# Kernel tuning notes

Hardware: AMD Instinct MI355X
Metric: run time of the kernel (lower is better)

The kernel has to match this reference:

```python
import jax, jax.numpy as jnp
import numpy as np

# dims
H = 1024          # hidden_size
E = 2048          # d_inner = 2*H
NH = 32           # nheads = E/64
P = 64            # headdim
N = 128           # d_state
G = 1             # ngroups
K = 4             # d_conv
Q = 128           # SSD chunk length
FF = 4096         # intermediate_size
EPS = 1e-6        # rms_norm_eps
NEPS = 1e-5       # mamba gated-norm eps
CONV_DIM = E + 2 * G * N            # 2304
D_IN = 2 * E + 2 * G * N + NH       # 4384


def rmsnorm(x, w, eps):
    v = jnp.mean(x.astype(jnp.float32) ** 2, axis=-1, keepdims=True)
    return (x.astype(jnp.float32) * jax.lax.rsqrt(v + eps)).astype(x.dtype) * w


def segsum(x):
    # x: [..., T] -> [..., T, T] with out[i,j] = sum_{j<k<=i} x[k], -inf above diag
    T = x.shape[-1]
    cs = jnp.cumsum(x, axis=-1)
    s = cs[..., :, None] - cs[..., None, :]
    mask = jnp.tril(jnp.ones((T, T), dtype=bool))
    return jnp.where(mask, s, -jnp.inf)


def ssd(x, dt, A_log, B, C):
    # x:[b,l,nh,p], dt:[b,l,nh], B,C:[b,l,N] (ngroups=1, shared over heads)
    b, l, nh, p = x.shape
    A = -jnp.exp(A_log)                      # [nh]
    dA = dt * A                              # [b,l,nh]
    xd = x * dt[..., None]                   # discretized input
    c = l // Q
    xd = xd.reshape(b, c, Q, nh, p)
    dAc = dA.reshape(b, c, Q, nh).transpose(0, 3, 1, 2)   # [b,h,c,q]
    Bc = B.reshape(b, c, Q, N)
    Cc = C.reshape(b, c, Q, N)
    A_cs = jnp.cumsum(dAc, axis=-1)                        # [b,h,c,q]
    Lm = jnp.exp(segsum(dAc))                              # [b,h,c,q,q]
    # intra-chunk (diagonal blocks)
    Y_diag = jnp.einsum('bcqn,bcsn,bhcqs,bcshp->bcqhp', Cc, Bc, Lm, xd)
    # per-chunk final states
    decay_states = jnp.exp(A_cs[..., -1:] - A_cs)          # [b,h,c,q]
    states = jnp.einsum('bcqn,bhcq,bcqhp->bchpn', Bc, decay_states, xd)
    # inter-chunk recurrence (initial state = 0)
    A_last = jnp.pad(A_cs[..., -1], ((0, 0), (0, 0), (1, 0)))   # [b,h,c+1]
    decay_chunk = jnp.exp(segsum(A_last))                       # [b,h,c+1,c+1]
    states = jnp.concatenate([jnp.zeros_like(states[:, :1]), states], axis=1)
    new_states = jnp.einsum('bhzc,bchpn->bzhpn', decay_chunk, states)[:, :-1]
    Y_off = jnp.einsum('bcqn,bchpn,bhcq->bcqhp', Cc, new_states, jnp.exp(A_cs))
    return (Y_diag + Y_off).reshape(b, l, nh, p)


def mamba2(h, w_in, w_conv, b_conv, dt_bias, A_log, D, w_mnorm, w_out):
    b, l, _ = h.shape
    zxbcdt = h @ w_in.T                         # [b,l,D_IN]
    z, xBC, dt = jnp.split(zxbcdt, [E, E + CONV_DIM], axis=-1)
    # causal depthwise conv (kernel K) over channels of xBC
    pad = jnp.pad(xBC, ((0, 0), (K - 1, 0), (0, 0)))
    xBC = sum(pad[:, k:k + l, :] * w_conv[:, k] for k in range(K)) + b_conv
    xBC = jax.nn.silu(xBC)
    x, B, C = jnp.split(xBC, [E, E + G * N], axis=-1)
    dt = jax.nn.softplus(dt + dt_bias)          # [b,l,NH]
    xh = x.reshape(b, l, NH, P)
    y = ssd(xh, dt, A_log, B, C)
    y = y + D[None, None, :, None] * xh         # per-head skip
    y = y.reshape(b, l, E)
    y = rmsnorm(y * jax.nn.silu(z), w_mnorm, NEPS)   # gated RMSNorm
    return y @ w_out.T


def setup_inputs() -> dict:
    key = jax.random.key(0)
    ks = jax.random.split(key, 12)
    dt0 = jax.random.uniform(ks[0], (NH,), minval=0.001, maxval=0.1)
    dt_bias = dt0 + jnp.log(-jnp.expm1(-dt0))   # inverse softplus
    return {
        'hidden_states': jax.random.normal(ks[1], (2, 2048, H), dtype=jnp.float32),
        'w_ln1': jnp.ones((H,), jnp.float32),
        'w_in': 0.02 * jax.random.normal(ks[2], (D_IN, H), dtype=jnp.float32),
        'w_conv': 0.1 * jax.random.normal(ks[3], (CONV_DIM, K), dtype=jnp.float32),
        'b_conv': jnp.zeros((CONV_DIM,), jnp.float32),
        'dt_bias': dt_bias,
        'A_log': jnp.log(jax.random.uniform(ks[4], (NH,), minval=1.0, maxval=16.0)),
        'D': jnp.ones((NH,), jnp.float32),
        'w_mnorm': jnp.ones((E,), jnp.float32),
        'w_out': 0.02 * jax.random.normal(ks[5], (H, E), dtype=jnp.float32),
        'w_ln2': jnp.ones((H,), jnp.float32),
        'w_gate': 0.02 * jax.random.normal(ks[6], (FF, H), dtype=jnp.float32),
        'w_up': 0.02 * jax.random.normal(ks[7], (FF, H), dtype=jnp.float32),
        'w_down': 0.02 * jax.random.normal(ks[8], (H, FF), dtype=jnp.float32),
    }


def reference(hidden_states, w_ln1, w_in, w_conv, b_conv, dt_bias, A_log, D,
              w_mnorm, w_out, w_ln2, w_gate, w_up, w_down):
    residual = hidden_states
    h = rmsnorm(hidden_states, w_ln1, EPS)
    h = mamba2(h, w_in, w_conv, b_conv, dt_bias, A_log, D, w_mnorm, w_out)
    hidden = residual + h
    residual = hidden
    h = rmsnorm(hidden, w_ln2, EPS)
    h = (jax.nn.silu(h @ w_gate.T) * (h @ w_up.T)) @ w_down.T
    return residual + h
```

## Files before the change

kernel.cpp:

```cpp
#include <hip/hip_runtime.h>

#define DEV static __device__ __forceinline__

typedef short bf16x8 __attribute__((ext_vector_type(8)));
typedef float floatx4 __attribute__((ext_vector_type(4)));
typedef unsigned short ushort4v __attribute__((ext_vector_type(4)));
typedef unsigned short ushort8v __attribute__((ext_vector_type(8)));

DEV unsigned short f32_bf16(float f) {
  unsigned int u = __builtin_bit_cast(unsigned int, f);
  u = u + 0x7fffu + ((u >> 16) & 1u);
  return (unsigned short)(u >> 16);
}
DEV float bf2f(unsigned short u) {
  unsigned int v = ((unsigned int)u) << 16;
  return __builtin_bit_cast(float, v);
}
DEV float sigmoidf_(float x) { return 1.0f / (1.0f + __expf(-x)); }
DEV float siluf_(float x) { return x * sigmoidf_(x); }

#define GLD_LDS16(g, l)                                                              \
  __builtin_amdgcn_global_load_lds((const __attribute__((address_space(1))) void*)(g), \
                                   (__attribute__((address_space(3))) void*)(l), 16, 0, 0)

template <int MODE, int BN>
__global__ __launch_bounds__(256) void gemm128(
    const unsigned short* __restrict__ A, const unsigned short* __restrict__ B,
    void* __restrict__ Cv, const unsigned short* __restrict__ other,
    int K, int lda, int ldb, int ldc, long long bsA, long long bsB, long long bsC) {
  constexpr int NBG = BN / 64;
  constexpr int NJ = BN / 32;
  constexpr int BUFSZ = 4096 + BN * 32;
  __shared__ unsigned short S[3 * BUFSZ];
  A += (long long)blockIdx.z * bsA;
  B += (long long)blockIdx.z * bsB;
  const long long coff = (long long)blockIdx.z * bsC;
  const int tid = threadIdx.x;
  const int w = tid >> 6, lane = tid & 63;

  const int nbx = gridDim.x, nby = gridDim.y;
  const int GM = 4;
  int bid = blockIdx.y * nbx + blockIdx.x;
  int gid = bid / (GM * nbx);
  int rem = bid - gid * (GM * nbx);
  int gsz = min(GM, nby - gid * GM);
  int mtile = gid * GM + rem % gsz;
  int ntile = rem / gsz;
  const int m0 = mtile << 7, n0 = ntile * BN;

  const int srow = lane >> 2;
  const int schunk = ((lane & 3) ^ (srow & 3)) * 8;
  const unsigned short* ag0 = A + (long long)(m0 + w * 32 + srow) * lda + schunk;
  const unsigned short* ag1 = ag0 + (long long)16 * lda;
  const unsigned short* bgp[NBG];
#pragma unroll
  for (int ii = 0; ii < NBG; ++ii)
    bgp[ii] = B + (long long)(n0 + w * (BN / 4) + srow + 16 * ii) * ldb + schunk;

  auto STAGE = [&](int buf, int k0) {
    unsigned short* as_ = S + buf * BUFSZ;
    unsigned short* bs_ = as_ + 4096;
    GLD_LDS16(ag0 + k0, as_ + w * 1024 + lane * 8);
    GLD_LDS16(ag1 + k0, as_ + w * 1024 + lane * 8 + 512);
#pragma unroll
    for (int ii = 0; ii < NBG; ++ii)
      GLD_LDS16(bgp[ii] + k0, bs_ + w * (NBG * 512) + ii * 512 + lane * 8);
  };

  const int wr = (w >> 1) << 6;
  const int wc = (w & 1) * (BN / 2);
  const int fr = lane & 15;
  const int slot = (((lane >> 4) ^ (fr & 3))) << 3;
  const int r0 = (lane >> 4) << 2;

  floatx4 acc[4][NJ];
#pragma unroll
  for (int i = 0; i < 4; ++i)
#pragma unroll
    for (int j = 0; j < NJ; ++j) acc[i][j] = (floatx4){0.f, 0.f, 0.f, 0.f};

  const int nsteps = K >> 5;
  STAGE(0, 0);
  if (nsteps > 1) STAGE(1, 32);

  int cur = 0, nxt2 = 2;
  for (int t = 0; t < nsteps; ++t) {
    if (t < nsteps - 1) {
      if constexpr (NBG == 2) {
        asm volatile("s_waitcnt vmcnt(4)" ::: "memory");
      } else {
        asm volatile("s_waitcnt vmcnt(6)" ::: "memory");
      }
    } else {
      asm volatile("s_waitcnt vmcnt(0)" ::: "memory");
    }
    __builtin_amdgcn_s_barrier();
    __builtin_amdgcn_sched_barrier(0);
    if (t + 2 < nsteps) STAGE(nxt2, (t + 2) * 32);
    __builtin_amdgcn_sched_barrier(0);
    const unsigned short* Ab = S + cur * BUFSZ;
    const unsigned short* Bb = Ab + 4096;
    bf16x8 af[4], bf_[NJ];
#pragma unroll
    for (int i = 0; i < 4; ++i)
      af[i] = *(const bf16x8*)(Ab + (wr + i * 16 + fr) * 32 + slot);
#pragma unroll
    for (int j = 0; j < NJ; ++j)
      bf_[j] = *(const bf16x8*)(Bb + (wc + j * 16 + fr) * 32 + slot);
#pragma unroll
    for (int i = 0; i < 4; ++i)
#pragma unroll
      for (int j = 0; j < NJ; ++j)
        acc[i][j] = __builtin_amdgcn_mfma_f32_16x16x32_bf16(af[i], bf_[j], acc[i][j], 0, 0, 0);
    __builtin_amdgcn_sched_barrier(0);
    cur = (cur == 2) ? 0 : cur + 1;
    nxt2 = (nxt2 == 2) ? 0 : nxt2 + 1;
  }

  if constexpr (MODE == 0) {
#pragma unroll
    for (int i = 0; i < 4; ++i) {
#pragma unroll
      for (int j = 0; j < NJ; ++j) {
        long long base = (long long)(m0 + wr + i * 16 + r0) * ldc + (n0 + wc + j * 16 + fr);
#pragma unroll
        for (int r = 0; r < 4; ++r) {
          ((float*)Cv)[coff + base + (long long)r * ldc] = acc[i][j][r];
        }
      }
    }
  } else {
    constexpr int PAD = BN + 4;
    float* scr = (float*)S;
    const int row_l = tid >> 2;
    const int cch = (tid & 3) * 16;
    __syncthreads();
#pragma unroll
    for (int pass = 0; pass < 2; ++pass) {
      if ((w >> 1) == pass) {
#pragma unroll
        for (int i = 0; i < 4; ++i) {
#pragma unroll
          for (int j = 0; j < NJ; ++j) {
            int rl = i * 16 + r0;
            int col = wc + j * 16 + fr;
#pragma unroll
            for (int r = 0; r < 4; ++r) scr[(rl + r) * PAD + col] = acc[i][j][r];
          }
        }
      }
      __syncthreads();
      long long grow = m0 + pass * 64 + row_l;
      long long gbase = coff + grow * ldc + n0;
      const float* srow_p = scr + row_l * PAD;
#pragma unroll
      for (int k = 0; k < BN / 64; ++k) {
        int col = cch + k * 64;
        float v[16];
        *(float4*)&v[0] = *(const float4*)(srow_p + col);
        *(float4*)&v[4] = *(const float4*)(srow_p + col + 4);
        *(float4*)&v[8] = *(const float4*)(srow_p + col + 8);
        *(float4*)&v[12] = *(const float4*)(srow_p + col + 12);
        ushort8v o0, o1;
        if constexpr (MODE == 2) {
          ushort8v u0 = *(const ushort8v*)(other + gbase + col);
          ushort8v u1 = *(const ushort8v*)(other + gbase + col + 8);
#pragma unroll
          for (int e = 0; e < 8; ++e) o0[e] = f32_bf16(siluf_(v[e]) * bf2f(u0[e]));
#pragma unroll
          for (int e = 0; e < 8; ++e) o1[e] = f32_bf16(siluf_(v[8 + e]) * bf2f(u1[e]));
        } else {
#pragma unroll
          for (int e = 0; e < 8; ++e) o0[e] = f32_bf16(v[e]);
#pragma unroll
          for (int e = 0; e < 8; ++e) o1[e] = f32_bf16(v[8 + e]);
        }
        *(ushort8v*)((unsigned short*)Cv + gbase + col) = o0;
        *(ushort8v*)((unsigned short*)Cv + gbase + col + 8) = o1;
      }
      __syncthreads();
    }
  }
}

template <int WM>
__global__ __launch_bounds__(256) void gemm_small_nt(
    const unsigned short* __restrict__ A, const unsigned short* __restrict__ B,
    float* __restrict__ C, int M, int N, int K, int lda, int ldb, int ldc) {
  const int w = threadIdx.x >> 6;
  const int lane = threadIdx.x & 63;
  const int lm = lane & 15;
  const int ko = (lane >> 4) << 3;
  const int bn0 = blockIdx.x << 6;
  const int m_base = blockIdx.y * (WM * 64) + w * (WM * 16);

  const unsigned short* arow[WM];
#pragma unroll
  for (int i = 0; i < WM; ++i) arow[i] = A + (long long)(m_base + i * 16 + lm) * lda + ko;
  int nv = (N - bn0) >> 4;
  nv = nv > 4 ? 4 : nv;
  const unsigned short* brow[4];
#pragma unroll
  for (int j = 0; j < 4; ++j) {
    int nr = bn0 + j * 16 + lm;
    brow[j] = B + (long long)(j < nv ? nr : 0) * ldb + ko;
  }
  floatx4 acc[WM][4];
#pragma unroll
  for (int i = 0; i < WM; ++i)
#pragma unroll
    for (int j = 0; j < 4; ++j) acc[i][j] = (floatx4){0.f, 0.f, 0.f, 0.f};
  for (int k0 = 0; k0 < K; k0 += 32) {
    bf16x8 a[WM];
#pragma unroll
    for (int i = 0; i < WM; ++i) a[i] = *(const bf16x8*)(arow[i] + k0);
#pragma unroll
    for (int j = 0; j < 4; ++j) {
      if (j < nv) {
        bf16x8 b = *(const bf16x8*)(brow[j] + k0);
#pragma unroll
        for (int i = 0; i < WM; ++i)
          acc[i][j] = __builtin_amdgcn_mfma_f32_16x16x32_bf16(a[i], b, acc[i][j], 0, 0, 0);
      }
    }
  }
  const int r0 = (lane >> 4) << 2;
#pragma unroll
  for (int i = 0; i < WM; ++i)
#pragma unroll
    for (int j = 0; j < 4; ++j)
      if (j < nv) {
        int col = bn0 + j * 16 + lm;
        long long base = (long long)(m_base + i * 16 + r0) * ldc + col;
#pragma unroll
        for (int r = 0; r < 4; ++r) C[base + (long long)r * ldc] = acc[i][j][r];
      }
}

__global__ __launch_bounds__(256) void f32_to_bf16_k(const float* __restrict__ src,
                                                     unsigned short* __restrict__ dst,
                                                     long long n4) {
  long long i = (long long)blockIdx.x * 256 + threadIdx.x;
  if (i < n4) {
    float4 v = ((const float4*)src)[i];
    ushort4v o = {f32_bf16(v.x), f32_bf16(v.y), f32_bf16(v.z), f32_bf16(v.w)};
    ((ushort4v*)dst)[i] = o;
  }
}

__global__ __launch_bounds__(256) void zero_out_k(float* __restrict__ o, long long n) {
  long long i = (long long)blockIdx.x * 256 + threadIdx.x;
  if (i < n) o[i] = 0.f;
}

__global__ __launch_bounds__(256) void rmsnorm1024_bf16_k(const float* __restrict__ x,
                                                          const float* __restrict__ w,
                                                          unsigned short* __restrict__ out,
                                                          float eps) {
  long long row = blockIdx.x;
  int t = threadIdx.x;
  float4 v = ((const float4*)(x + row * 1024))[t];
  float ss = v.x * v.x + v.y * v.y + v.z * v.z + v.w * v.w;
  __shared__ float red[4];
#pragma unroll
  for (int o = 32; o > 0; o >>= 1) ss += __shfl_down(ss, o, 64);
  if ((t & 63) == 0) red[t >> 6] = ss;
  __syncthreads();
  float tot = red[0] + red[1] + red[2] + red[3];
  float sc = rsqrtf(tot * (1.0f / 1024.0f) + eps);
  float4 wv = ((const float4*)w)[t];
  ushort4v o = {f32_bf16(v.x * sc * wv.x), f32_bf16(v.y * sc * wv.y),
                f32_bf16(v.z * sc * wv.z), f32_bf16(v.w * sc * wv.w)};
  ((ushort4v*)(out + row * 1024))[t] = o;
}

__global__ __launch_bounds__(256) void add_rmsnorm_k(const float* __restrict__ hs,
                                                     const float* __restrict__ parts,
                                                     long long pstride, int np,
                                                     const float* __restrict__ w,
                                                     float* __restrict__ mh,
                                                     unsigned short* __restrict__ h2, float eps) {
  long long row = blockIdx.x;
  int t = threadIdx.x;
  float4 v = ((const float4*)(hs + row * 1024))[t];
  for (int p = 0; p < np; ++p) {
    float4 u = ((const float4*)(parts + p * pstride + row * 1024))[t];
    v.x += u.x;
    v.y += u.y;
    v.z += u.z;
    v.w += u.w;
  }
  ((float4*)(mh + row * 1024))[t] = v;
  float ss = v.x * v.x + v.y * v.y + v.z * v.z + v.w * v.w;
  __shared__ float red[4];
#pragma unroll
  for (int o = 32; o > 0; o >>= 1) ss += __shfl_down(ss, o, 64);
  if ((t & 63) == 0) red[t >> 6] = ss;
  __syncthreads();
  float tot = red[0] + red[1] + red[2] + red[3];
  float sc = rsqrtf(tot * (1.0f / 1024.0f) + eps);
  float4 wv = ((const float4*)w)[t];
  ushort4v o = {f32_bf16(v.x * sc * wv.x), f32_bf16(v.y * sc * wv.y),
                f32_bf16(v.z * sc * wv.z), f32_bf16(v.w * sc * wv.w)};
  ((ushort4v*)(h2 + row * 1024))[t] = o;
}

__global__ __launch_bounds__(256) void addn_f32_k(const float* __restrict__ a,
                                                  const float* __restrict__ parts,
                                                  long long pstride, int np,
                                                  float* __restrict__ o, long long n4) {
  long long i = (long long)blockIdx.x * 256 + threadIdx.x;
  if (i < n4) {
    float4 x = ((const float4*)a)[i];
    for (int p = 0; p < np; ++p) {
      float4 u = ((const float4*)(parts + p * pstride))[i];
      x.x += u.x;
      x.y += u.y;
      x.z += u.z;
      x.w += u.w;
    }
    ((float4*)o)[i] = x;
  }
}

__global__ __launch_bounds__(256) void gated_rmsnorm2048_k(const unsigned short* __restrict__ y,
                                                           const unsigned short* __restrict__ z,
                                                           const float* __restrict__ w,
                                                           unsigned short* __restrict__ out,
                                                           float eps) {
  long long row = blockIdx.x;
  int t = threadIdx.x;
  ushort8v yv = ((const ushort8v*)(y + row * 2048))[t];
  ushort8v zv = ((const ushort8v*)(z + row * 2048))[t];
  float g[8];
  float ss = 0.f;
#pragma unroll
  for (int j = 0; j < 8; ++j) {
    g[j] = bf2f(yv[j]) * siluf_(bf2f(zv[j]));
    ss += g[j] * g[j];
  }
  __shared__ float red[4];
#pragma unroll
  for (int o = 32; o > 0; o >>= 1) ss += __shfl_down(ss, o, 64);
  if ((t & 63) == 0) red[t >> 6] = ss;
  __syncthreads();
  float tot = red[0] + red[1] + red[2] + red[3];
  float sc = rsqrtf(tot * (1.0f / 2048.0f) + eps);
  float ww[8];
  *(float4*)&ww[0] = ((const float4*)w)[2 * t];
  *(float4*)&ww[4] = ((const float4*)w)[2 * t + 1];
  ushort8v o;
#pragma unroll
  for (int j = 0; j < 8; ++j) o[j] = f32_bf16(g[j] * sc * ww[j]);
  ((ushort8v*)(out + row * 2048))[t] = o;
}

__global__ __launch_bounds__(256) void conv_silu_k(const unsigned short* __restrict__ xraw,
                                                   const float* __restrict__ wconv,
                                                   const float* __restrict__ bconv,
                                                   unsigned short* __restrict__ xBC) {
  int m = blockIdx.x;
  int l = m & 2047;
  for (int cb = threadIdx.x; cb < 288; cb += 256) {
    int ch0 = cb << 3;
    float acc[8];
    float4 bc0 = ((const float4*)bconv)[cb * 2];
    float4 bc1 = ((const float4*)bconv)[cb * 2 + 1];
    acc[0] = bc0.x; acc[1] = bc0.y; acc[2] = bc0.z; acc[3] = bc0.w;
    acc[4] = bc1.x; acc[5] = bc1.y; acc[6] = bc1.z; acc[7] = bc1.w;
    float4 wv[8];
#pragma unroll
    for (int j = 0; j < 8; ++j) wv[j] = ((const float4*)wconv)[ch0 + j];
#pragma unroll
    for (int k = 0; k < 4; ++k) {
      int lk = l + k - 3;
      if (lk >= 0) {
        ushort8v xv = *(const ushort8v*)(xraw + (long long)(m + k - 3) * 2304 + ch0);
        acc[0] += bf2f(xv[0]) * ((const float*)&wv[0])[k];
        acc[1] += bf2f(xv[1]) * ((const float*)&wv[1])[k];
        acc[2] += bf2f(xv[2]) * ((const float*)&wv[2])[k];
        acc[3] += bf2f(xv[3]) * ((const float*)&wv[3])[k];
        acc[4] += bf2f(xv[4]) * ((const float*)&wv[4])[k];
        acc[5] += bf2f(xv[5]) * ((const float*)&wv[5])[k];
        acc[6] += bf2f(xv[6]) * ((const float*)&wv[6])[k];
        acc[7] += bf2f(xv[7]) * ((const float*)&wv[7])[k];
      }
    }
    ushort8v o;
#pragma unroll
    for (int j = 0; j < 8; ++j) o[j] = f32_bf16(siluf_(acc[j]));
    *(ushort8v*)(xBC + (long long)m * 2304 + ch0) = o;
  }
}

__global__ __launch_bounds__(256) void dt_softplus_k(const float* __restrict__ dtraw,
                                                     const float* __restrict__ dt_bias,
                                                     float* __restrict__ dt_s) {
  int i = blockIdx.x * 256 + threadIdx.x;
  float xv = dtraw[i] + dt_bias[i & 31];
  dt_s[i] = xv > 20.f ? xv : log1pf(expf(xv));
}

__global__ __launch_bounds__(128) void dA_cumsum_k(const float* __restrict__ dt_s,
                                                   const float* __restrict__ A_log,
                                                   float* __restrict__ dA_cs) {
  int bi = blockIdx.x;
  int c = bi & 15, h = (bi >> 4) & 31, b = bi >> 9;
  int q = threadIdx.x;
  float A = -expf(A_log[h]);
  float v = dt_s[((long long)(b * 2048 + c * 128 + q)) * 32 + h] * A;
  __shared__ float sbuf[128];
  sbuf[q] = v;
  __syncthreads();
  for (int off = 1; off < 128; off <<= 1) {
    float tv = (q >= off) ? sbuf[q - off] : 0.f;
    __syncthreads();
    sbuf[q] += tv;
    __syncthreads();
  }
  dA_cs[(long long)bi * 128 + q] = sbuf[q];
}

__global__ __launch_bounds__(256) void ssd_diag_states_k(
    const unsigned short* __restrict__ xBC, const float* __restrict__ dt_s,
    const float* __restrict__ dA_cs, const unsigned short* __restrict__ G,
    unsigned short* __restrict__ y, unsigned short* __restrict__ states) {
  __shared__ unsigned short Mz[128 * 136];
  __shared__ unsigned short xdT[64 * 136];
  __shared__ float Acs[128];
  __shared__ float wdec[128];
  const int bx = blockIdx.x;
  const int h = bx & 31, c = (bx >> 5) & 15, b = bx >> 9;
  const int t = threadIdx.x;
  const int w = t >> 6, lane = t & 63, fr = lane & 15, hi = lane >> 4;
  const long long rowbase = (long long)b * 2048 + c * 128;
  const long long abase = ((long long)((b * 32 + h) * 16 + c)) << 7;

  if (t < 128) {
    float a = dA_cs[abase + t];
    Acs[t] = a;
    wdec[t] = __expf(dA_cs[abase + 127] - a);
  }
  {
    int s = t >> 1, p0 = (t & 1) * 32;
    float dtv = dt_s[(rowbase + s) * 32 + h];
    const ushort8v* xv = (const ushort8v*)(xBC + (rowbase + s) * 2304 + h * 64 + p0);
#pragma unroll
    for (int i = 0; i < 4; ++i) {
      ushort8v vv = xv[i];
#pragma unroll
      for (int j = 0; j < 8; ++j) xdT[(p0 + i * 8 + j) * 136 + s] = f32_bf16(bf2f(vv[j]) * dtv);
    }
  }
  __syncthreads();
  {
    int q = t >> 1, s0 = (t & 1) * 64;
    float aq = Acs[q];
    const ushort8v* gv =
        (const ushort8v*)(G + (((long long)(b * 16 + c)) * 128 + q) * 128 + s0);
#pragma unroll
    for (int i = 0; i < 8; ++i) {
      ushort8v gg = gv[i];
#pragma unroll
      for (int j = 0; j < 8; ++j) {
        int s = s0 + i * 8 + j;
        float m = (s <= q) ? bf2f(gg[j]) * __expf(aq - Acs[s]) : 0.f;
        Mz[q * 136 + s] = f32_bf16(m);
      }
    }
  }
  __syncthreads();
  const int q0 = w << 5;
  {
    floatx4 acc[2][4];
#pragma unroll
    for (int i = 0; i < 2; ++i)
#pragma unroll
      for (int j = 0; j < 4; ++j) acc[i][j] = (floatx4){0.f, 0.f, 0.f, 0.f};
#pragma unroll
    for (int k0 = 0; k0 < 128; k0 += 32) {
      int kk = k0 + hi * 8;
      bf16x8 a0 = *(const bf16x8*)(Mz + (q0 + fr) * 136 + kk);
      bf16x8 a1 = *(const bf16x8*)(Mz + (q0 + 16 + fr) * 136 + kk);
      bf16x8 bf_[4];
#pragma unroll
      for (int j = 0; j < 4; ++j) bf_[j] = *(const bf16x8*)(xdT + (j * 16 + fr) * 136 + kk);
#pragma unroll
      for (int j = 0; j < 4; ++j) {
        acc[0][j] = __builtin_amdgcn_mfma_f32_16x16x32_bf16(a0, bf_[j], acc[0][j], 0, 0, 0);
        acc[1][j] = __builtin_amdgcn_mfma_f32_16x16x32_bf16(a1, bf_[j], acc[1][j], 0, 0, 0);
      }
    }
#pragma unroll
    for (int i = 0; i < 2; ++i)
#pragma unroll
      for (int r = 0; r < 4; ++r) {
        int q = q0 + i * 16 + hi * 4 + r;
        unsigned short* yrow = y + (rowbase + q) * 2048 + h * 64;
#pragma unroll
        for (int j = 0; j < 4; ++j) yrow[j * 16 + fr] = f32_bf16(acc[i][j][r]);
      }
  }
  __syncthreads();
  {
    int s = t >> 1, n0 = (t & 1) * 64;
    float wd = wdec[s];
    const ushort8v* bv = (const ushort8v*)(xBC + (rowbase + s) * 2304 + 2048 + n0);
#pragma unroll
    for (int i = 0; i < 8; ++i) {
      ushort8v bb = bv[i];
#pragma unroll
      for (int j = 0; j < 8; ++j) Mz[(n0 + i * 8 + j) * 136 + s] = f32_bf16(bf2f(bb[j]) * wd);
    }
  }
  __syncthreads();
  {
    floatx4 acc[2][4];
#pragma unroll
    for (int i = 0; i < 2; ++i)
#pragma unroll
      for (int j = 0; j < 4; ++j) acc[i][j] = (floatx4){0.f, 0.f, 0.f, 0.f};
#pragma unroll
    for (int k0 = 0; k0 < 128; k0 += 32) {
      int kk = k0 + hi * 8;
      bf16x8 a0 = *(const bf16x8*)(Mz + (q0 + fr) * 136 + kk);
      bf16x8 a1 = *(const bf16x8*)(Mz + (q0 + 16 + fr) * 136 + kk);
      bf16x8 bf_[4];
#pragma unroll
      for (int j = 0; j < 4; ++j) bf_[j] = *(const bf16x8*)(xdT + (j * 16 + fr) * 136 + kk);
#pragma unroll
      for (int j = 0; j < 4; ++j) {
        acc[0][j] = __builtin_amdgcn_mfma_f32_16x16x32_bf16(a0, bf_[j], acc[0][j], 0, 0, 0);
        acc[1][j] = __builtin_amdgcn_mfma_f32_16x16x32_bf16(a1, bf_[j], acc[1][j], 0, 0, 0);
      }
    }
    unsigned short* st = states + (long long)bx * 8192;
#pragma unroll
    for (int i = 0; i < 2; ++i)
#pragma unroll
      for (int j = 0; j < 4; ++j) {
        int p = j * 16 + fr;
        int n = q0 + i * 16 + hi * 4;
        ushort4v o;
#pragma unroll
        for (int r = 0; r < 4; ++r) o[r] = f32_bf16(acc[i][j][r]);
        *(ushort4v*)(st + p * 128 + n) = o;
      }
  }
}

__global__ __launch_bounds__(256) void ssd_scan_k(const float* __restrict__ dA_cs,
                                                  unsigned short* __restrict__ states) {
  int seg = blockIdx.x & 7;
  int h = (blockIdx.x >> 3) & 31;
  int b = blockIdx.x >> 8;
  int t = threadIdx.x;
  int e0 = seg * 1024 + t;
  float carry[4];
#pragma unroll
  for (int i = 0; i < 4; ++i) carry[i] = 0.f;
  for (int c = 0; c < 16; ++c) {
    long long base = ((long long)((b * 16 + c) * 32 + h)) * 8192;
    float dec = __expf(dA_cs[(((long long)((b * 32 + h) * 16 + c)) << 7) + 127]);
#pragma unroll
    for (int i = 0; i < 4; ++i) {
      long long idx = base + e0 + i * 256;
      float local = bf2f(states[idx]);
      states[idx] = f32_bf16(carry[i]);
      carry[i] = dec * carry[i] + local;
    }
  }
}

__global__ __launch_bounds__(256) void ssd_off_k(const unsigned short* __restrict__ xBC,
                                                 const float* __restrict__ dA_cs,
                                                 const unsigned short* __restrict__ states,
                                                 const float* __restrict__ Dvec,
                                                 unsigned short* __restrict__ y) {
  __shared__ float eA[128];
  const int bx = blockIdx.x;
  const int h = bx & 31, c = (bx >> 5) & 15, b = bx >> 9;
  const int t = threadIdx.x;
  const int w = t >> 6, lane = t & 63, fr = lane & 15, hi = lane >> 4;
  const long long rowbase = (long long)b * 2048 + c * 128;
  const long long abase = ((long long)((b * 32 + h) * 16 + c)) << 7;
  if (t < 128) eA[t] = __expf(dA_cs[abase + t]);
  __syncthreads();

  const unsigned short* st = states + (long long)bx * 8192;
  const int q0 = w << 5;
  floatx4 acc[2][4];
#pragma unroll
  for (int i = 0; i < 2; ++i)
#pragma unroll
    for (int j = 0; j < 4; ++j) acc[i][j] = (floatx4){0.f, 0.f, 0.f, 0.f};

#pragma unroll
  for (int k0 = 0; k0 < 128; k0 += 32) {
    int kk = k0 + hi * 8;
    bf16x8 a0 = *(const bf16x8*)(xBC + (rowbase + q0 + fr) * 2304 + 2176 + kk);
    bf16x8 a1 = *(const bf16x8*)(xBC + (rowbase + q0 + 16 + fr) * 2304 + 2176 + kk);
    bf16x8 bf_[4];
#pragma unroll
    for (int j = 0; j < 4; ++j) bf_[j] = *(const bf16x8*)(st + (j * 16 + fr) * 128 + kk);
#pragma unroll
    for (int j = 0; j < 4; ++j) {
      acc[0][j] = __builtin_amdgcn_mfma_f32_16x16x32_bf16(a0, bf_[j], acc[0][j], 0, 0, 0);
      acc[1][j] = __builtin_amdgcn_mfma_f32_16x16x32_bf16(a1, bf_[j], acc[1][j], 0, 0, 0);
    }
  }

  float Dh = Dvec[h];
#pragma unroll
  for (int i = 0; i < 2; ++i) {
#pragma unroll
    for (int r = 0; r < 4; ++r) {
      int q = q0 + i * 16 + hi * 4 + r;
      float e = eA[q];
      const unsigned short* xrow = xBC + (rowbase + q) * 2304 + h * 64;
      unsigned short* yrow = y + (rowbase + q) * 2048 + h * 64;
#pragma unroll
      for (int j = 0; j < 4; ++j) {
        int p = j * 16 + fr;
        float v = bf2f(yrow[p]) + e * acc[i][j][r] + Dh * bf2f(xrow[p]);
        yrow[p] = f32_bf16(v);
      }
    }
  }
}

extern "C" void kernel_launch(void* const* d_in, const int* in_sizes, int n_in, void* d_out,
                              int out_size, void* d_ws, size_t ws_size, hipStream_t stream) {
  const float* hs = (const float*)d_in[0];
  const float* w_ln1 = (const float*)d_in[1];
  const float* w_in = (const float*)d_in[2];
  const float* w_conv = (const float*)d_in[3];
  const float* b_conv = (const float*)d_in[4];
  const float* dt_bias = (const float*)d_in[5];
  const float* A_log = (const float*)d_in[6];
  const float* Dvec = (const float*)d_in[7];
  const float* w_mnorm = (const float*)d_in[8];
  const float* w_out = (const float*)d_in[9];
  const float* w_ln2 = (const float*)d_in[10];
  const float* w_gate = (const float*)d_in[11];
  const float* w_up = (const float*)d_in[12];
  const float* w_down = (const float*)d_in[13];
  float* out = (float*)d_out;
  const int M = 4096;

  char* ws = (char*)d_ws;
  const size_t R0 = 0;
  const size_t R1 = 33554432;
  const size_t R1b = R1 + 33554432;
  const size_t R2 = 71303168;
  const size_t R3 = 90177536;
  const size_t R4 = 107544576;
  const size_t W0 = 108068864;
  const size_t NEED = 133234688;

  if (ws_size < NEED) {
    hipLaunchKernelGGL(zero_out_k, dim3((out_size + 255) / 256), dim3(256), 0, stream, out,
                       (long long)out_size);
    return;
  }

  unsigned short* z = (unsigned short*)(ws + R0);
  unsigned short* act = (unsigned short*)(ws + R0);
  float* oproj_parts = (float*)(ws + R0);
  unsigned short* xraw = (unsigned short*)(ws + R1);
  unsigned short* states = (unsigned short*)(ws + R1);
  unsigned short* ybuf = (unsigned short*)(ws + R1 + 16777216);
  unsigned short* upo = (unsigned short*)(ws + R1);
  float* down_parts = (float*)(ws + R1);
  unsigned short* wbf_out = (unsigned short*)(ws + R1b);
  unsigned short* xBC = (unsigned short*)(ws + R2);
  unsigned short* ygn = (unsigned short*)(ws + R2);
  unsigned short* h2 = (unsigned short*)(ws + R2);
  unsigned short* hnorm = (unsigned short*)(ws + R3);
  unsigned short* wbf_in = (unsigned short*)(ws + R3 + 8388608);
  float* dt_s = (float*)(ws + R3);
  float* dA_cs = (float*)(ws + R3 + 524288);
  unsigned short* Gbuf = (unsigned short*)(ws + R3 + 1048576);
  float* mh = (float*)(ws + R3);
  float* dtraw = (float*)(ws + R4);
  unsigned short* wbf_gate = (unsigned short*)(ws + W0);
  unsigned short* wbf_up = (unsigned short*)(ws + W0 + 8388608);
  unsigned short* wbf_down = (unsigned short*)(ws + W0 + 16777216);

  hipLaunchKernelGGL(rmsnorm1024_bf16_k, dim3(M), dim3(256), 0, stream, hs, w_ln1, hnorm, 1e-6f);
  hipLaunchKernelGGL(f32_to_bf16_k, dim3(4384), dim3(256), 0, stream, w_in, wbf_in, 1122304LL);
  hipLaunchKernelGGL(f32_to_bf16_k, dim3(4096), dim3(256), 0, stream, w_gate, wbf_gate, 1048576LL);
  hipLaunchKernelGGL(f32_to_bf16_k, dim3(4096), dim3(256), 0, stream, w_up, wbf_up, 1048576LL);
  hipLaunchKernelGGL(f32_to_bf16_k, dim3(4096), dim3(256), 0, stream, w_down, wbf_down, 1048576LL);
  hipLaunchKernelGGL((gemm128<1, 256>), dim3(8, 32, 1), dim3(256), 0, stream, hnorm, wbf_in,
                     (void*)z, (const unsigned short*)nullptr, 1024, 1024, 1024, 2048, 0LL, 0LL,
                     0LL);
  hipLaunchKernelGGL((gemm128<1, 256>), dim3(9, 32, 1), dim3(256), 0, stream, hnorm,
                     wbf_in + 2048 * 1024, (void*)xraw, (const unsigned short*)nullptr, 1024, 1024,
                     1024, 2304, 0LL, 0LL, 0LL);
  hipLaunchKernelGGL((gemm_small_nt<4>), dim3(1, 16, 1), dim3(256), 0, stream, hnorm,
                     wbf_in + 4352 * 1024, dtraw, M, 32, 1024, 1024, 1024, 32);
  hipLaunchKernelGGL(conv_silu_k, dim3(M), dim3(256), 0, stream, xraw, w_conv, b_conv, xBC);
  hipLaunchKernelGGL(f32_to_bf16_k, dim3(2048), dim3(256), 0, stream, w_out, wbf_out, 524288LL);
  hipLaunchKernelGGL(dt_softplus_k, dim3(512), dim3(256), 0, stream, dtraw, dt_bias, dt_s);
  hipLaunchKernelGGL(dA_cumsum_k, dim3(1024), dim3(128), 0, stream, dt_s, A_log, dA_cs);
  hipLaunchKernelGGL((gemm128<1, 128>), dim3(1, 1, 32), dim3(256), 0, stream, xBC + 2176,
                     xBC + 2048, (void*)Gbuf, (const unsigned short*)nullptr, 128, 2304, 2304, 128,
                     294912LL, 294912LL, 16384LL);
  hipLaunchKernelGGL(ssd_diag_states_k, dim3(1024), dim3(256), 0, stream, xBC, dt_s, dA_cs, Gbuf,
                     ybuf, states);
  hipLaunchKernelGGL(ssd_scan_k, dim3(512), dim3(256), 0, stream, dA_cs, states);
  hipLaunchKernelGGL(ssd_off_k, dim3(1024), dim3(256), 0, stream, xBC, dA_cs, states, Dvec, ybuf);
  hipLaunchKernelGGL(gated_rmsnorm2048_k, dim3(M), dim3(256), 0, stream, ybuf, z, w_mnorm, ygn,
                     1e-5f);
  hipLaunchKernelGGL((gemm128<0, 256>), dim3(4, 32, 4), dim3(256), 0, stream, ygn, wbf_out,
                     (void*)oproj_parts, (const unsigned short*)nullptr, 512, 2048, 2048, 1024,
                     512LL, 512LL, 4194304LL);
  hipLaunchKernelGGL(add_rmsnorm_k, dim3(M), dim3(256), 0, stream, hs, oproj_parts, 4194304LL, 4,
                     w_ln2, mh, h2, 1e-6f);
  hipLaunchKernelGGL((gemm128<1, 256>), dim3(16, 32, 1), dim3(256), 0, stream, h2, wbf_up,
                     (void*)upo, (const unsigned short*)nullptr, 1024, 1024, 1024, 4096, 0LL, 0LL,
                     0LL);
  hipLaunchKernelGGL((gemm128<2, 256>), dim3(16, 32, 1), dim3(256), 0, stream, h2, wbf_gate,
                     (void*)act, upo, 1024, 1024, 1024, 4096, 0LL, 0LL, 0LL);
  hipLaunchKernelGGL((gemm128<0, 256>), dim3(4, 32, 2), dim3(256), 0, stream, act, wbf_down,
                     (void*)down_parts, (const unsigned short*)nullptr, 2048, 4096, 4096, 1024,
                     2048LL, 2048LL, 4194304LL);
  hipLaunchKernelGGL(addn_f32_k, dim3(4096), dim3(256), 0, stream, mh, down_parts, 4194304LL, 2,
                     out, 1048576LL);
}
```

Baseline: 575.1 us.

## Switch GEMM to double-buffered LDS and shrink epilogue scratch footprint

The GEMM main loop moves from triple-buffered shared memory to double buffering, with the next prefetch issued after a second barrier at the end of each step. This cuts LDS use per block, likely to fit more blocks per CU. The epilogue is restructured into four 32-row passes with 8-element chunks so the scratch stays within the smaller shared buffer. The out-projection split-K factor is also lowered from 4 to 2. The trade-off is less load/compute overlap and an extra barrier per k-step.

```diff
diff --git a/kernel.cpp b/kernel.cpp
--- a/kernel.cpp
+++ b/kernel.cpp
@@ -31,7 +31,7 @@
   constexpr int NBG = BN / 64;
   constexpr int NJ = BN / 32;
   constexpr int BUFSZ = 4096 + BN * 32;
-  __shared__ unsigned short S[3 * BUFSZ];
+  __shared__ unsigned short S[2 * BUFSZ];
   A += (long long)blockIdx.z * bsA;
   B += (long long)blockIdx.z * bsB;
   const long long coff = (long long)blockIdx.z * bsC;
@@ -83,7 +83,6 @@
   STAGE(0, 0);
   if (nsteps > 1) STAGE(1, 32);
 
-  int cur = 0, nxt2 = 2;
   for (int t = 0; t < nsteps; ++t) {
     if (t < nsteps - 1) {
       if constexpr (NBG == 2) {
@@ -96,9 +95,7 @@
     }
     __builtin_amdgcn_s_barrier();
     __builtin_amdgcn_sched_barrier(0);
-    if (t + 2 < nsteps) STAGE(nxt2, (t + 2) * 32);
-    __builtin_amdgcn_sched_barrier(0);
-    const unsigned short* Ab = S + cur * BUFSZ;
+    const unsigned short* Ab = S + (t & 1) * BUFSZ;
     const unsigned short* Bb = Ab + 4096;
     bf16x8 af[4], bf_[NJ];
 #pragma unroll
@@ -113,8 +110,8 @@
       for (int j = 0; j < NJ; ++j)
         acc[i][j] = __builtin_amdgcn_mfma_f32_16x16x32_bf16(af[i], bf_[j], acc[i][j], 0, 0, 0);
     __builtin_amdgcn_sched_barrier(0);
-    cur = (cur == 2) ? 0 : cur + 1;
-    nxt2 = (nxt2 == 2) ? 0 : nxt2 + 1;
+    __builtin_amdgcn_s_barrier();
+    if (t + 2 < nsteps) STAGE(t & 1, (t + 2) * 32);
   }
 
   if constexpr (MODE == 0) {
@@ -132,17 +129,18 @@
   } else {
     constexpr int PAD = BN + 4;
     float* scr = (float*)S;
-    const int row_l = tid >> 2;
-    const int cch = (tid & 3) * 16;
+    const int row_l = tid >> 3;
+    const int col0 = (tid & 7) * 8;
     __syncthreads();
 #pragma unroll
-    for (int pass = 0; pass < 2; ++pass) {
-      if ((w >> 1) == pass) {
-#pragma unroll
-        for (int i = 0; i < 4; ++i) {
+    for (int pass = 0; pass < 4; ++pass) {
+      if ((w >> 1) == (pass >> 1)) {
+#pragma unroll
+        for (int ii = 0; ii < 2; ++ii) {
+          int i = (pass & 1) * 2 + ii;
+          int rl = i * 16 + r0 - (pass & 1) * 32;
 #pragma unroll
           for (int j = 0; j < NJ; ++j) {
-            int rl = i * 16 + r0;
             int col = wc + j * 16 + fr;
 #pragma unroll
             for (int r = 0; r < 4; ++r) scr[(rl + r) * PAD + col] = acc[i][j][r];
@@ -150,33 +148,25 @@
         }
       }
       __syncthreads();
-      long long grow = m0 + pass * 64 + row_l;
+      long long grow = m0 + pass * 32 + row_l;
       long long gbase = coff + grow * ldc + n0;
       const float* srow_p = scr + row_l * PAD;
 #pragma unroll
       for (int k = 0; k < BN / 64; ++k) {
-        int col = cch + k * 64;
-        float v[16];
+        int col = col0 + k * 64;
+        float v[8];
         *(float4*)&v[0] = *(const float4*)(srow_p + col);
         *(float4*)&v[4] = *(const float4*)(srow_p + col + 4);
-        *(float4*)&v[8] = *(const float4*)(srow_p + col + 8);
-        *(float4*)&v[12] = *(const float4*)(srow_p + col + 12);
-        ushort8v o0, o1;
+        ushort8v o;
         if constexpr (MODE == 2) {
-          ushort8v u0 = *(const ushort8v*)(other + gbase + col);
-          ushort8v u1 = *(const ushort8v*)(other + gbase + col + 8);
-#pragma unroll
-          for (int e = 0; e < 8; ++e) o0[e] = f32_bf16(siluf_(v[e]) * bf2f(u0[e]));
-#pragma unroll
-          for (int e = 0; e < 8; ++e) o1[e] = f32_bf16(siluf_(v[8 + e]) * bf2f(u1[e]));
+          ushort8v uo = *(const ushort8v*)(other + gbase + col);
+#pragma unroll
+          for (int e = 0; e < 8; ++e) o[e] = f32_bf16(siluf_(v[e]) * bf2f(uo[e]));
         } else {
 #pragma unroll
-          for (int e = 0; e < 8; ++e) o0[e] = f32_bf16(v[e]);
-#pragma unroll
-          for (int e = 0; e < 8; ++e) o1[e] = f32_bf16(v[8 + e]);
+          for (int e = 0; e < 8; ++e) o[e] = f32_bf16(v[e]);
         }
-        *(ushort8v*)((unsigned short*)Cv + gbase + col) = o0;
-        *(ushort8v*)((unsigned short*)Cv + gbase + col + 8) = o1;
+        *(ushort8v*)((unsigned short*)Cv + gbase + col) = o;
       }
       __syncthreads();
     }
@@ -713,10 +703,10 @@
   hipLaunchKernelGGL(ssd_off_k, dim3(1024), dim3(256), 0, stream, xBC, dA_cs, states, Dvec, ybuf);
   hipLaunchKernelGGL(gated_rmsnorm2048_k, dim3(M), dim3(256), 0, stream, ybuf, z, w_mnorm, ygn,
                      1e-5f);
-  hipLaunchKernelGGL((gemm128<0, 256>), dim3(4, 32, 4), dim3(256), 0, stream, ygn, wbf_out,
-                     (void*)oproj_parts, (const unsigned short*)nullptr, 512, 2048, 2048, 1024,
-                     512LL, 512LL, 4194304LL);
-  hipLaunchKernelGGL(add_rmsnorm_k, dim3(M), dim3(256), 0, stream, hs, oproj_parts, 4194304LL, 4,
+  hipLaunchKernelGGL((gemm128<0, 256>), dim3(4, 32, 2), dim3(256), 0, stream, ygn, wbf_out,
+                     (void*)oproj_parts, (const unsigned short*)nullptr, 1024, 2048, 2048, 1024,
+                     1024LL, 1024LL, 4194304LL);
+  hipLaunchKernelGGL(add_rmsnorm_k, dim3(M), dim3(256), 0, stream, hs, oproj_parts, 4194304LL, 2,
                      w_ln2, mh, h2, 1e-6f);
   hipLaunchKernelGGL((gemm128<1, 256>), dim3(16, 32, 1), dim3(256), 0, stream, h2, wbf_up,
                      (void*)upo, (const unsigned short*)nullptr, 1024, 1024, 1024, 4096, 0LL, 0LL,
```

Measured after the change: 550.8 us. 1.04x faster.
